# Kernel optimization log

Measured on AMD Instinct MI355X. Metric: run time of the kernel, lower is better.

The kernel has to match this reference:

```python
import jax, jax.numpy as jnp
import numpy as np

N_NODES = 100000
N_EDGES = 1600000
D_IN = 64
D_OUT = 64


def setup_inputs() -> dict:
    key = jax.random.key(0)
    k1, k2, k3, k4 = jax.random.split(key, 4)
    feat = jax.random.normal(k1, (N_NODES, D_IN), dtype=jnp.float32)
    edge_src = jax.random.randint(k2, (N_EDGES,), 0, N_NODES, dtype=jnp.int64)
    edge_dst = jax.random.randint(k3, (N_EDGES,), 0, N_NODES, dtype=jnp.int64)
    # xavier_uniform with gain for relu (sqrt(2)) on [out, in] Linear weight
    gain = float(np.sqrt(2.0))
    limit = gain * float(np.sqrt(6.0 / (D_IN + D_OUT)))
    fc_weight = jax.random.uniform(k4, (D_OUT, D_IN), dtype=jnp.float32,
                                   minval=-limit, maxval=limit)
    return {"feat": feat, "edge_src": edge_src, "edge_dst": edge_dst,
            "fc_weight": fc_weight}


def reference(feat, edge_src, edge_dst, fc_weight):
    # SDDMM: edge score a_e = <h_src, h_dst>  (fn.u_dot_v)
    h_src = feat[edge_src]                      # [E, d]
    h_dst = feat[edge_dst]                      # [E, d]
    a = jnp.sum(h_src * h_dst, axis=-1, keepdims=True)  # [E, 1]
    # SpMM: neigh[v] = sum_{(u->v)} h_u * a_e  (u_mul_e + sum)
    m = h_src * a                               # [E, d]
    neigh = jax.ops.segment_sum(m, edge_dst, num_segments=feat.shape[0])  # [N, d]
    # Linear without bias: y = neigh @ W.T
    return neigh @ fc_weight.T
```

## Files before the change

### kernel.cpp

```cpp
#include <hip/hip_runtime.h>

#define N_NODES 100000
#define N_EDGES 1600000
#define D 64
#define NB 782
#define CAP 3072
#define EPB 8192
#define NPART ((N_EDGES + EPB - 1) / EPB)
#define RSH 14

typedef unsigned short ushort_t;
typedef unsigned int uint_t;

__device__ __forceinline__ ushort_t f2bf(float f) {
    uint_t u = __float_as_uint(f);
    u += 0x7FFF + ((u >> 16) & 1);
    return (ushort_t)(u >> 16);
}

__global__ __launch_bounds__(256) void repack_init(const float* __restrict__ feat,
                                                   ushort_t* __restrict__ featb,
                                                   int* __restrict__ gcur) {
    const int tid = blockIdx.x * 256 + threadIdx.x;
    if (tid < NB) gcur[tid] = tid * CAP;
    const int base = tid * 16;
    if (base >= N_NODES * D) return;
    const float4* f4 = (const float4*)(feat + base);
    ushort4* o4 = (ushort4*)(featb + base);
#pragma unroll
    for (int j = 0; j < 4; ++j) {
        const float4 v = f4[j];
        o4[j] = make_ushort4(f2bf(v.x), f2bf(v.y), f2bf(v.z), f2bf(v.w));
    }
}

__global__ __launch_bounds__(1024) void partition(const int* __restrict__ esrc,
                                                  const int* __restrict__ edst,
                                                  int* __restrict__ gcur,
                                                  int* __restrict__ slab) {
    __shared__ int stage[EPB];
    __shared__ ushort_t bkt16[EPB];
    __shared__ int cnt[NB];
    __shared__ int cur[NB];
    __shared__ int gb[NB];
    __shared__ int s[1024];
    const int t = threadIdx.x;
    const int base = blockIdx.x * EPB;
    const int n = min(EPB, N_EDGES - base);

    if (t < NB) cnt[t] = 0;
    __syncthreads();
    for (int i = t; i < n; i += 1024)
        atomicAdd(&cnt[edst[base + i] >> 7], 1);
    __syncthreads();
    const int v = (t < NB) ? cnt[t] : 0;
    s[t] = v;
    __syncthreads();
    for (int off = 1; off < 1024; off <<= 1) {
        const int x = (t >= off) ? s[t - off] : 0;
        __syncthreads();
        s[t] += x;
        __syncthreads();
    }
    if (t < NB) {
        const int excl = s[t] - v;
        cur[t] = excl;
        gb[t] = (v ? atomicAdd(&gcur[t], v) : 0) - excl;
    }
    __syncthreads();
    for (int i = t; i < n; i += 1024) {
        const int d = edst[base + i];
        const int bkt = d >> 7;
        const int pos = atomicAdd(&cur[bkt], 1);
        stage[pos] = ((d & 127) << 17) | esrc[base + i];
        bkt16[pos] = (ushort_t)bkt;
    }
    __syncthreads();
    for (int i = t; i < n; i += 1024) {
        const int bkt = bkt16[i];
        const int gp = gb[bkt] + i;
        if (gp < (bkt + 1) * CAP)
            slab[gp] = stage[i];
    }
}

template<int CTRL>
__device__ __forceinline__ float fadd_dpp(float x) {
    const int r = __builtin_amdgcn_update_dpp(0, __float_as_int(x), CTRL, 0xF, 0xF, true);
    return x + __int_as_float(r);
}
__device__ __forceinline__ float red8(float p) {
    p = fadd_dpp<0xB1>(p);
    p = fadd_dpp<0x4E>(p);
    p = fadd_dpp<0x141>(p);
    return p;
}

__device__ __forceinline__ void cvt8(const uint4 u, float* __restrict__ g) {
    g[0] = __uint_as_float(u.x << 16); g[1] = __uint_as_float(u.x & 0xFFFF0000u);
    g[2] = __uint_as_float(u.y << 16); g[3] = __uint_as_float(u.y & 0xFFFF0000u);
    g[4] = __uint_as_float(u.z << 16); g[5] = __uint_as_float(u.z & 0xFFFF0000u);
    g[6] = __uint_as_float(u.w << 16); g[7] = __uint_as_float(u.w & 0xFFFF0000u);
}
__device__ __forceinline__ float cvt_dot(const uint4 u, const float* __restrict__ h,
                                         float* __restrict__ g) {
    cvt8(u, g);
    float p = 0.f;
#pragma unroll
    for (int k = 0; k < 8; ++k) p += g[k] * h[k];
    return p;
}

__global__ __launch_bounds__(512) void fused_spmm_gemm(
    const uint4* __restrict__ featb4,
    const int* __restrict__ slab,
    const int* __restrict__ gcur,
    const float* __restrict__ W,
    float* __restrict__ out)
{
    __shared__ __align__(16) char ovl[32768];
    __shared__ int seB[CAP];
    __shared__ int rowoff[129];
    int* seA     = (int*)ovl;
    int* kcnt    = (int*)(ovl + 12288);
    int* kcur    = (int*)(ovl + 16384);
    int* s       = (int*)(ovl + 20480);
    float* accs  = (float*)ovl;
    float4* accs4 = (float4*)ovl;

    const int t = threadIdx.x;
    const int b = blockIdx.x;
    const int nbase = b << 7;
    const int nb_nodes = min(128, N_NODES - nbase);
    const int sbase = b * CAP;
    const int ne = min(gcur[b] - sbase, CAP);

    for (int i = t; i < ne; i += 512) seA[i] = slab[sbase + i];
    kcnt[t] = 0; kcnt[t + 512] = 0;
    __syncthreads();
    for (int i = t; i < ne; i += 512) {
        const int pk = seA[i];
        atomicAdd(&kcnt[((pk >> 17) << 3) | ((pk & 0x1FFFF) >> RSH)], 1);
    }
    __syncthreads();
    const int v0 = kcnt[2 * t], v1 = kcnt[2 * t + 1];
    const int sum = v0 + v1;
    s[t] = sum;
    __syncthreads();
    for (int off = 1; off < 512; off <<= 1) {
        const int x = (t >= off) ? s[t - off] : 0;
        __syncthreads();
        s[t] += x;
        __syncthreads();
    }
    const int excl = s[t] - sum;
    kcur[2 * t] = excl;
    kcur[2 * t + 1] = excl + v0;
    __syncthreads();
    if (t < 128) rowoff[t] = kcur[t << 3];
    if (t == 0) rowoff[128] = ne;
    __syncthreads();
    for (int i = t; i < ne; i += 512) {
        const int pk = seA[i];
        const int key = ((pk >> 17) << 3) | ((pk & 0x1FFFF) >> RSH);
        const int pos = atomicAdd(&kcur[key], 1);
        seB[pos] = pk & 0x1FFFF;
    }
    __syncthreads();

    const int slot = t >> 3;
    const int l = t & 7;
#pragma unroll
    for (int ln0 = 0; ln0 < 128; ln0 += 64) {
        const int ln = ln0 + slot;
        if (ln >= nb_nodes) continue;
        const int nidx = nbase + ln;
        float h[8];
        cvt8(featb4[nidx * 8 + l], h);
        float acc[8];
#pragma unroll
        for (int k = 0; k < 8; ++k) acc[k] = 0.f;

        int e = rowoff[ln];
        const int e1 = rowoff[ln + 1];
        for (; e + 3 < e1; e += 4) {
            const int s0 = seB[e], s1 = seB[e + 1], s2 = seB[e + 2], s3 = seB[e + 3];
            const uint4 u0 = featb4[s0 * 8 + l];
            const uint4 u1 = featb4[s1 * 8 + l];
            const uint4 u2 = featb4[s2 * 8 + l];
            const uint4 u3 = featb4[s3 * 8 + l];
            float g0[8], g1[8], g2[8], g3[8];
            float p0 = cvt_dot(u0, h, g0);
            float p1 = cvt_dot(u1, h, g1);
            float p2 = cvt_dot(u2, h, g2);
            float p3 = cvt_dot(u3, h, g3);
            p0 = red8(p0); p1 = red8(p1); p2 = red8(p2); p3 = red8(p3);
#pragma unroll
            for (int k = 0; k < 8; ++k)
                acc[k] += g0[k] * p0 + g1[k] * p1 + g2[k] * p2 + g3[k] * p3;
        }
        for (; e < e1; ++e) {
            const uint4 u0 = featb4[seB[e] * 8 + l];
            float g0[8];
            float p0 = red8(cvt_dot(u0, h, g0));
#pragma unroll
            for (int k = 0; k < 8; ++k) acc[k] += g0[k] * p0;
        }
        accs4[ln * 16 + 2 * l]     = make_float4(acc[0], acc[1], acc[2], acc[3]);
        accs4[ln * 16 + 2 * l + 1] = make_float4(acc[4], acc[5], acc[6], acc[7]);
    }
    __syncthreads();

    const int o = t & 63;
    const int rg = t >> 6;
    float wcol[D];
    {
        const float4* W4 = (const float4*)(W + o * D);
#pragma unroll
        for (int i4 = 0; i4 < 16; ++i4) {
            const float4 w = W4[i4];
            wcol[4 * i4 + 0] = w.x; wcol[4 * i4 + 1] = w.y;
            wcol[4 * i4 + 2] = w.z; wcol[4 * i4 + 3] = w.w;
        }
    }
    for (int r = rg; r < nb_nodes; r += 8) {
        const float4* arow = (const float4*)&accs[r * D];
        float sumv = 0.f;
#pragma unroll
        for (int i4 = 0; i4 < 16; ++i4) {
            const float4 a4 = arow[i4];
            sumv += a4.x * wcol[4 * i4 + 0];
            sumv += a4.y * wcol[4 * i4 + 1];
            sumv += a4.z * wcol[4 * i4 + 2];
            sumv += a4.w * wcol[4 * i4 + 3];
        }
        out[(nbase + r) * D + o] = sumv;
    }
}

extern "C" void kernel_launch(void* const* d_in, const int* in_sizes, int n_in,
                              void* d_out, int out_size, void* d_ws, size_t ws_size,
                              hipStream_t stream) {
    const float* feat = (const float*)d_in[0];
    const int*   esrc = (const int*)d_in[1];
    const int*   edst = (const int*)d_in[2];
    const float* W    = (const float*)d_in[3];
    float* out = (float*)d_out;

    char* ws = (char*)d_ws;
    ushort_t* featb = (ushort_t*)(ws);
    int* slab = (int*)(ws + 12800000);
    int* gcur = (int*)(ws + 12800000 + (size_t)NB * CAP * 4);

    repack_init<<<(N_NODES * D / 16 + 255) / 256, 256, 0, stream>>>(feat, featb, gcur);
    partition<<<NPART, 1024, 0, stream>>>(esrc, edst, gcur, slab);
    fused_spmm_gemm<<<NB, 512, 0, stream>>>((const uint4*)featb, slab, gcur, W, out);
}
```

Baseline: 203.0 us.

## Merge repack into partition kernel, simplify bucket sort, tile register-blocked GEMM epilogue

Folds the bf16 feature repack and the edge partition into one launch, using extra blocks for the repack, and replaces the gcur init with a memset. Partition blocks shrink to 4096 edges with 512 threads. The per-row source-range sub-bucketing in the SpMM kernel is dropped in favour of a plain 128-bucket sort by row. The final 64x64 GEMM now stages transposed W in padded shared memory and computes 4x4 register tiles per thread with vectorised stores. This removes a launch and cuts LDS and scan work, but it gives up the source-locality ordering of gathers within each row.

Result: slower. 470.9 us (+132.0%).

```diff
diff --git a/kernel.cpp b/kernel.cpp
--- a/kernel.cpp
+++ b/kernel.cpp
@@ -5,9 +5,9 @@
 #define D 64
 #define NB 782
 #define CAP 3072
-#define EPB 8192
-#define NPART ((N_EDGES + EPB - 1) / EPB)
-#define RSH 14
+#define EPB 4096
+#define NPART 391
+#define NREPACK 782
 
 typedef unsigned short ushort_t;
 typedef unsigned int uint_t;
@@ -18,57 +18,67 @@
     return (ushort_t)(u >> 16);
 }
 
-__global__ __launch_bounds__(256) void repack_init(const float* __restrict__ feat,
+__global__ __launch_bounds__(512) void part_repack(const float* __restrict__ feat,
                                                    ushort_t* __restrict__ featb,
-                                                   int* __restrict__ gcur) {
-    const int tid = blockIdx.x * 256 + threadIdx.x;
-    if (tid < NB) gcur[tid] = tid * CAP;
-    const int base = tid * 16;
-    if (base >= N_NODES * D) return;
-    const float4* f4 = (const float4*)(feat + base);
-    ushort4* o4 = (ushort4*)(featb + base);
-#pragma unroll
-    for (int j = 0; j < 4; ++j) {
-        const float4 v = f4[j];
-        o4[j] = make_ushort4(f2bf(v.x), f2bf(v.y), f2bf(v.z), f2bf(v.w));
-    }
-}
-
-__global__ __launch_bounds__(1024) void partition(const int* __restrict__ esrc,
-                                                  const int* __restrict__ edst,
-                                                  int* __restrict__ gcur,
-                                                  int* __restrict__ slab) {
+                                                   const int* __restrict__ esrc,
+                                                   const int* __restrict__ edst,
+                                                   int* __restrict__ gcur,
+                                                   int* __restrict__ slab) {
     __shared__ int stage[EPB];
     __shared__ ushort_t bkt16[EPB];
     __shared__ int cnt[NB];
     __shared__ int cur[NB];
     __shared__ int gb[NB];
-    __shared__ int s[1024];
+    __shared__ int s[512];
     const int t = threadIdx.x;
+
+    if (blockIdx.x >= NPART) {
+        const int idx = (blockIdx.x - NPART) * 512 + t;
+        const int base = idx * 16;
+        if (base < N_NODES * D) {
+            const float4* f4 = (const float4*)(feat + base);
+            ushort4* o4 = (ushort4*)(featb + base);
+#pragma unroll
+            for (int j = 0; j < 4; ++j) {
+                const float4 v = f4[j];
+                o4[j] = make_ushort4(f2bf(v.x), f2bf(v.y), f2bf(v.z), f2bf(v.w));
+            }
+        }
+        return;
+    }
+
     const int base = blockIdx.x * EPB;
     const int n = min(EPB, N_EDGES - base);
 
-    if (t < NB) cnt[t] = 0;
-    __syncthreads();
-    for (int i = t; i < n; i += 1024)
+    for (int i = t; i < NB; i += 512) cnt[i] = 0;
+    __syncthreads();
+    for (int i = t; i < n; i += 512)
         atomicAdd(&cnt[edst[base + i] >> 7], 1);
     __syncthreads();
-    const int v = (t < NB) ? cnt[t] : 0;
-    s[t] = v;
-    __syncthreads();
-    for (int off = 1; off < 1024; off <<= 1) {
+    int c0 = 0, c1 = 0;
+    if (2 * t < NB) c0 = cnt[2 * t];
+    if (2 * t + 1 < NB) c1 = cnt[2 * t + 1];
+    const int sum = c0 + c1;
+    s[t] = sum;
+    __syncthreads();
+    for (int off = 1; off < 512; off <<= 1) {
         const int x = (t >= off) ? s[t - off] : 0;
         __syncthreads();
         s[t] += x;
         __syncthreads();
     }
-    if (t < NB) {
-        const int excl = s[t] - v;
-        cur[t] = excl;
-        gb[t] = (v ? atomicAdd(&gcur[t], v) : 0) - excl;
-    }
-    __syncthreads();
-    for (int i = t; i < n; i += 1024) {
+    int run = s[t] - sum;
+    if (2 * t < NB) {
+        cur[2*t] = run;
+        gb[2*t] = (c0 ? atomicAdd(&gcur[2*t], c0) : 0) + (2*t)*CAP - run;
+        run += c0;
+    }
+    if (2 * t + 1 < NB) {
+        cur[2*t+1] = run;
+        gb[2*t+1] = (c1 ? atomicAdd(&gcur[2*t+1], c1) : 0) + (2*t+1)*CAP - run;
+    }
+    __syncthreads();
+    for (int i = t; i < n; i += 512) {
         const int d = edst[base + i];
         const int bkt = d >> 7;
         const int pos = atomicAdd(&cur[bkt], 1);
@@ -76,7 +86,7 @@
         bkt16[pos] = (ushort_t)bkt;
     }
     __syncthreads();
-    for (int i = t; i < n; i += 1024) {
+    for (int i = t; i < n; i += 512) {
         const int bkt = bkt16[i];
         const int gp = gb[bkt] + i;
         if (gp < (bkt + 1) * CAP)
@@ -110,6 +120,8 @@
     for (int k = 0; k < 8; ++k) p += g[k] * h[k];
     return p;
 }
+
+#define APITCH 68
 
 __global__ __launch_bounds__(512) void fused_spmm_gemm(
     const uint4* __restrict__ featb4,
@@ -118,52 +130,62 @@
     const float* __restrict__ W,
     float* __restrict__ out)
 {
-    __shared__ __align__(16) char ovl[32768];
+    __shared__ __align__(16) char ovl[128 * APITCH * 4];
     __shared__ int seB[CAP];
+    __shared__ float WT[64][APITCH];
     __shared__ int rowoff[129];
-    int* seA     = (int*)ovl;
-    int* kcnt    = (int*)(ovl + 12288);
-    int* kcur    = (int*)(ovl + 16384);
-    int* s       = (int*)(ovl + 20480);
-    float* accs  = (float*)ovl;
-    float4* accs4 = (float4*)ovl;
+    int* seA   = (int*)ovl;
+    int* kcnt  = (int*)(ovl + 12288);
+    int* kcur  = (int*)(ovl + 14336);
+    int* s     = (int*)(ovl + 16384);
+    float* accs = (float*)ovl;
 
     const int t = threadIdx.x;
     const int b = blockIdx.x;
     const int nbase = b << 7;
     const int nb_nodes = min(128, N_NODES - nbase);
     const int sbase = b * CAP;
-    const int ne = min(gcur[b] - sbase, CAP);
+    const int ne = min(gcur[b], CAP);
+
+    {
+        const float4* W4 = (const float4*)W;
+#pragma unroll
+        for (int j = 0; j < 2; ++j) {
+            const int f = t + j * 512;
+            const int o = f >> 4;
+            const int i4 = (f & 15) * 4;
+            const float4 w = W4[f];
+            WT[i4 + 0][o] = w.x;
+            WT[i4 + 1][o] = w.y;
+            WT[i4 + 2][o] = w.z;
+            WT[i4 + 3][o] = w.w;
+        }
+    }
 
     for (int i = t; i < ne; i += 512) seA[i] = slab[sbase + i];
-    kcnt[t] = 0; kcnt[t + 512] = 0;
+    if (t < 128) kcnt[t] = 0;
+    __syncthreads();
+    for (int i = t; i < ne; i += 512)
+        atomicAdd(&kcnt[seA[i] >> 17], 1);
+    __syncthreads();
+    const int v = (t < 128) ? kcnt[t] : 0;
+    s[t] = v;
+    __syncthreads();
+    for (int off = 1; off < 128; off <<= 1) {
+        const int x = (t >= off) ? s[t - off] : 0;
+        __syncthreads();
+        s[t] += x;
+        __syncthreads();
+    }
+    if (t < 128) {
+        rowoff[t] = s[t] - v;
+        kcur[t] = s[t] - v;
+    }
+    if (t == 0) rowoff[128] = ne;
     __syncthreads();
     for (int i = t; i < ne; i += 512) {
         const int pk = seA[i];
-        atomicAdd(&kcnt[((pk >> 17) << 3) | ((pk & 0x1FFFF) >> RSH)], 1);
-    }
-    __syncthreads();
-    const int v0 = kcnt[2 * t], v1 = kcnt[2 * t + 1];
-    const int sum = v0 + v1;
-    s[t] = sum;
-    __syncthreads();
-    for (int off = 1; off < 512; off <<= 1) {
-        const int x = (t >= off) ? s[t - off] : 0;
-        __syncthreads();
-        s[t] += x;
-        __syncthreads();
-    }
-    const int excl = s[t] - sum;
-    kcur[2 * t] = excl;
-    kcur[2 * t + 1] = excl + v0;
-    __syncthreads();
-    if (t < 128) rowoff[t] = kcur[t << 3];
-    if (t == 0) rowoff[128] = ne;
-    __syncthreads();
-    for (int i = t; i < ne; i += 512) {
-        const int pk = seA[i];
-        const int key = ((pk >> 17) << 3) | ((pk & 0x1FFFF) >> RSH);
-        const int pos = atomicAdd(&kcur[key], 1);
+        const int pos = atomicAdd(&kcur[pk >> 17], 1);
         seB[pos] = pk & 0x1FFFF;
     }
     __syncthreads();
@@ -173,68 +195,74 @@
 #pragma unroll
     for (int ln0 = 0; ln0 < 128; ln0 += 64) {
         const int ln = ln0 + slot;
-        if (ln >= nb_nodes) continue;
-        const int nidx = nbase + ln;
-        float h[8];
-        cvt8(featb4[nidx * 8 + l], h);
-        float acc[8];
-#pragma unroll
-        for (int k = 0; k < 8; ++k) acc[k] = 0.f;
-
-        int e = rowoff[ln];
-        const int e1 = rowoff[ln + 1];
-        for (; e + 3 < e1; e += 4) {
-            const int s0 = seB[e], s1 = seB[e + 1], s2 = seB[e + 2], s3 = seB[e + 3];
-            const uint4 u0 = featb4[s0 * 8 + l];
-            const uint4 u1 = featb4[s1 * 8 + l];
-            const uint4 u2 = featb4[s2 * 8 + l];
-            const uint4 u3 = featb4[s3 * 8 + l];
-            float g0[8], g1[8], g2[8], g3[8];
-            float p0 = cvt_dot(u0, h, g0);
-            float p1 = cvt_dot(u1, h, g1);
-            float p2 = cvt_dot(u2, h, g2);
-            float p3 = cvt_dot(u3, h, g3);
-            p0 = red8(p0); p1 = red8(p1); p2 = red8(p2); p3 = red8(p3);
-#pragma unroll
-            for (int k = 0; k < 8; ++k)
-                acc[k] += g0[k] * p0 + g1[k] * p1 + g2[k] * p2 + g3[k] * p3;
-        }
-        for (; e < e1; ++e) {
-            const uint4 u0 = featb4[seB[e] * 8 + l];
-            float g0[8];
-            float p0 = red8(cvt_dot(u0, h, g0));
-#pragma unroll
-            for (int k = 0; k < 8; ++k) acc[k] += g0[k] * p0;
-        }
-        accs4[ln * 16 + 2 * l]     = make_float4(acc[0], acc[1], acc[2], acc[3]);
-        accs4[ln * 16 + 2 * l + 1] = make_float4(acc[4], acc[5], acc[6], acc[7]);
-    }
-    __syncthreads();
-
-    const int o = t & 63;
-    const int rg = t >> 6;
-    float wcol[D];
-    {
-        const float4* W4 = (const float4*)(W + o * D);
-#pragma unroll
-        for (int i4 = 0; i4 < 16; ++i4) {
-            const float4 w = W4[i4];
-            wcol[4 * i4 + 0] = w.x; wcol[4 * i4 + 1] = w.y;
-            wcol[4 * i4 + 2] = w.z; wcol[4 * i4 + 3] = w.w;
-        }
-    }
-    for (int r = rg; r < nb_nodes; r += 8) {
-        const float4* arow = (const float4*)&accs[r * D];
-        float sumv = 0.f;
-#pragma unroll
-        for (int i4 = 0; i4 < 16; ++i4) {
-            const float4 a4 = arow[i4];
-            sumv += a4.x * wcol[4 * i4 + 0];
-            sumv += a4.y * wcol[4 * i4 + 1];
-            sumv += a4.z * wcol[4 * i4 + 2];
-            sumv += a4.w * wcol[4 * i4 + 3];
-        }
-        out[(nbase + r) * D + o] = sumv;
+        if (ln < nb_nodes) {
+            const int nidx = nbase + ln;
+            float h[8];
+            cvt8(featb4[nidx * 8 + l], h);
+            float acc[8];
+#pragma unroll
+            for (int k = 0; k < 8; ++k) acc[k] = 0.f;
+
+            int e = rowoff[ln];
+            const int e1 = rowoff[ln + 1];
+            for (; e + 3 < e1; e += 4) {
+                const int s0 = seB[e], s1 = seB[e+1], s2 = seB[e+2], s3 = seB[e+3];
+                const uint4 u0 = featb4[s0 * 8 + l];
+                const uint4 u1 = featb4[s1 * 8 + l];
+                const uint4 u2 = featb4[s2 * 8 + l];
+                const uint4 u3 = featb4[s3 * 8 + l];
+                float g0[8], g1[8], g2[8], g3[8];
+                float p0 = cvt_dot(u0, h, g0);
+                float p1 = cvt_dot(u1, h, g1);
+                float p2 = cvt_dot(u2, h, g2);
+                float p3 = cvt_dot(u3, h, g3);
+                p0 = red8(p0); p1 = red8(p1); p2 = red8(p2); p3 = red8(p3);
+#pragma unroll
+                for (int k = 0; k < 8; ++k)
+                    acc[k] += g0[k] * p0 + g1[k] * p1 + g2[k] * p2 + g3[k] * p3;
+            }
+            for (; e < e1; ++e) {
+                const uint4 u0 = featb4[seB[e] * 8 + l];
+                float g0[8];
+                float p0 = red8(cvt_dot(u0, h, g0));
+#pragma unroll
+                for (int k = 0; k < 8; ++k) acc[k] += g0[k] * p0;
+            }
+            *(float4*)&accs[ln * APITCH + 8 * l]     = make_float4(acc[0], acc[1], acc[2], acc[3]);
+            *(float4*)&accs[ln * APITCH + 8 * l + 4] = make_float4(acc[4], acc[5], acc[6], acc[7]);
+        }
+    }
+    __syncthreads();
+
+    const int c4 = (t & 15) * 4;
+    const int r0 = (t >> 4) * 4;
+    float acc[4][4];
+#pragma unroll
+    for (int r = 0; r < 4; ++r)
+#pragma unroll
+        for (int c = 0; c < 4; ++c) acc[r][c] = 0.f;
+
+    for (int i4 = 0; i4 < 16; ++i4) {
+        const int i = i4 * 4;
+        const float4 w0 = *(const float4*)&WT[i + 0][c4];
+        const float4 w1 = *(const float4*)&WT[i + 1][c4];
+        const float4 w2 = *(const float4*)&WT[i + 2][c4];
+        const float4 w3 = *(const float4*)&WT[i + 3][c4];
+#pragma unroll
+        for (int r = 0; r < 4; ++r) {
+            const float4 a = *(const float4*)&accs[(r0 + r) * APITCH + i];
+            acc[r][0] += a.x * w0.x + a.y * w1.x + a.z * w2.x + a.w * w3.x;
+            acc[r][1] += a.x * w0.y + a.y * w1.y + a.z * w2.y + a.w * w3.y;
+            acc[r][2] += a.x * w0.z + a.y * w1.z + a.z * w2.z + a.w * w3.z;
+            acc[r][3] += a.x * w0.w + a.y * w1.w + a.z * w2.w + a.w * w3.w;
+        }
+    }
+#pragma unroll
+    for (int r = 0; r < 4; ++r) {
+        const int rr = r0 + r;
+        if (rr < nb_nodes)
+            *(float4*)&out[(long)(nbase + rr) * D + c4] =
+                make_float4(acc[r][0], acc[r][1], acc[r][2], acc[r][3]);
     }
 }
 
@@ -252,7 +280,7 @@
     int* slab = (int*)(ws + 12800000);
     int* gcur = (int*)(ws + 12800000 + (size_t)NB * CAP * 4);
 
-    repack_init<<<(N_NODES * D / 16 + 255) / 256, 256, 0, stream>>>(feat, featb, gcur);
-    partition<<<NPART, 1024, 0, stream>>>(esrc, edst, gcur, slab);
+    hipMemsetAsync(gcur, 0, NB * sizeof(int), stream);
+    part_repack<<<NPART + NREPACK, 512, 0, stream>>>(feat, featb, esrc, edst, gcur, slab);
     fused_spmm_gemm<<<NB, 512, 0, stream>>>((const uint4*)featb, slab, gcur, W, out);
 }
```
